# Optimization experiments

Hardware: AMD Instinct MI355X
Metric: run time of the kernel (lower is better)

Reference implementation:

```python
import jax, jax.numpy as jnp
import numpy as np

B, C, P, D = 8192, 1000, 8, 512

def setup_inputs() -> dict:
    key = jax.random.key(0)
    kz, km = jax.random.split(key)
    z = jax.random.normal(kz, (B, D), dtype=jnp.float32)
    mu = jax.random.normal(km, (C, P, D), dtype=jnp.float32)
    return {"z": z, "mu": mu}

def reference(z, mu):
    # Squared Euclidean distance via the GEMM expansion:
    # ||z - mu||^2 = ||z||^2 - 2 z.mu + ||mu||^2  -> [B, C, P]
    z2 = jnp.sum(z * z, axis=-1)          # [B]
    mu2 = jnp.sum(mu * mu, axis=-1)       # [C, P]
    cross = jnp.einsum('bd,cpd->bcp', z, mu)  # [B, C, P]
    dist_sq = z2[:, None, None] - 2.0 * cross + mu2[None, :, :]
    min_dist_sq = jnp.min(dist_sq, axis=2)    # [B, C]
    logits = -min_dist_sq
    return (logits, min_dist_sq)
```

## Files before the change

kernel.cpp:

```cpp
#include <hip/hip_runtime.h>
#include <hip/hip_bf16.h>
#include <stdint.h>
#include <stddef.h>

#define B_ROWS 8192
#define C_CLS  1000
#define NPROTO 8000
#define D_DIM  512

#define TK 64
#define MT 32
#define NT 32

typedef __bf16 bf16x8 __attribute__((ext_vector_type(8)));
typedef float  f32x4  __attribute__((ext_vector_type(4)));

#define AS1 __attribute__((address_space(1)))
#define AS3 __attribute__((address_space(3)))

__device__ __forceinline__ void gload_lds16(const void* g, void* l) {
  __builtin_amdgcn_global_load_lds((const AS1 uint32_t*)g, (AS3 uint32_t*)l, 16, 0, 0);
}

__device__ __forceinline__ f32x4 mfma16(bf16x8 a, bf16x8 b, f32x4 c) {
  return __builtin_amdgcn_mfma_f32_16x16x32_bf16(a, b, c, 0, 0, 0);
}

#define ABUF(d) ((d) * 65536)
#define BBUF(d) ((d) * 65536 + 32768)
#define Z2OFF   131072
#define MU2OFF  132096
#define LDS_BYTES 133120

__global__ void prep_rows(const float* __restrict__ z, const float* __restrict__ mu,
                          __bf16* __restrict__ zb, __bf16* __restrict__ mub,
                          float* __restrict__ z2, float* __restrict__ mu2) {
  const int r = blockIdx.x * 4 + (threadIdx.x >> 6);
  const int l = threadIdx.x & 63;
  const float* src; __bf16* dst; float* sq; int row;
  if (r < B_ROWS) { src = z;  dst = zb;  sq = z2;  row = r; }
  else            { src = mu; dst = mub; sq = mu2; row = r - B_ROWS; }
  const float4* s4 = (const float4*)(src + (size_t)row * D_DIM);
  float4 v0 = s4[l * 2], v1 = s4[l * 2 + 1];
  float ss = v0.x * v0.x + v0.y * v0.y + v0.z * v0.z + v0.w * v0.w
           + v1.x * v1.x + v1.y * v1.y + v1.z * v1.z + v1.w * v1.w;
  bf16x8 o;
  o[0] = (__bf16)v0.x; o[1] = (__bf16)v0.y; o[2] = (__bf16)v0.z; o[3] = (__bf16)v0.w;
  o[4] = (__bf16)v1.x; o[5] = (__bf16)v1.y; o[6] = (__bf16)v1.z; o[7] = (__bf16)v1.w;
  ((bf16x8*)(dst + (size_t)row * D_DIM))[l] = o;
  #pragma unroll
  for (int off = 32; off; off >>= 1) ss += __shfl_down(ss, off);
  if (l == 0) sq[row] = ss;
}

__launch_bounds__(512, 2)
__global__ void proto_gemm(const __bf16* __restrict__ Zb, const __bf16* __restrict__ Mub,
                           const float* __restrict__ Z2, const float* __restrict__ Mu2,
                           float* __restrict__ logits, float* __restrict__ mind) {
  __shared__ __align__(16) unsigned char smem[LDS_BYTES];

  const int tid = threadIdx.x;
  const int l   = tid & 63;
  const int w   = tid >> 6;
  const int wm  = w >> 2;
  const int wn  = w & 3;

  const int xcd = blockIdx.x & 7, cc = blockIdx.x >> 3;
  const int mt = (xcd & 1) * 16 + (cc >> 3);
  const int nt = (xcd >> 1) * 8 + (cc & 7);

  const int sr   = tid >> 3;
  const int scol = ((tid & 7) * 8) ^ ((sr & 7) * 8);
  const __bf16* pA[4]; const __bf16* pB[4];
  #pragma unroll
  for (int q = 0; q < 4; ++q) {
    int rp = mt * 256 + q * 64 + sr;
    if (rp > NPROTO - 1) rp = NPROTO - 1;
    pA[q] = Mub + (size_t)rp * D_DIM + scol;
    pB[q] = Zb + (size_t)(nt * 256 + q * 64 + sr) * D_DIM + scol;
  }
  const int ldst = tid * 16;

  #define STAGE(T, D)                                                        \
    {                                                                        \
      _Pragma("unroll")                                                      \
      for (int q = 0; q < 4; ++q)                                            \
        gload_lds16(pA[q] + (T) * TK, smem + ABUF(D) + q * 8192 + ldst);     \
      _Pragma("unroll")                                                      \
      for (int q = 0; q < 4; ++q)                                            \
        gload_lds16(pB[q] + (T) * TK, smem + BBUF(D) + q * 8192 + ldst);     \
    }

  STAGE(0, 0);
  STAGE(1, 1);

  float* z2s  = (float*)(smem + Z2OFF);
  float* mu2s = (float*)(smem + MU2OFF);
  if (tid < 256) {
    z2s[tid] = Z2[nt * 256 + tid];
  } else {
    const int i = tid - 256;
    const int gp = mt * 256 + i;
    mu2s[i] = Mu2[gp < NPROTO ? gp : NPROTO - 1];
  }

  const int lx = (l & 7) << 4;
  const int lane_lin = (l & 15) * 128 + (l >> 4) * 16;
  const int ok0 = lane_lin ^ lx;
  const int ok1 = (lane_lin + 64) ^ lx;
  const int abase_w = wm * 16384;
  const int bbase_w = wn * 8192;

  f32x4 acc[8][4];
  #pragma unroll
  for (int i = 0; i < 8; ++i)
    #pragma unroll
    for (int j = 0; j < 4; ++j) acc[i][j] = (f32x4){0.f, 0.f, 0.f, 0.f};

  asm volatile("s_waitcnt vmcnt(8)" ::: "memory");
  __builtin_amdgcn_s_barrier();

  #define KTILE(T, DOSTAGE, VMEND)                                               \
  {                                                                              \
    constexpr int d_ = (T) & 1;                                                  \
    const unsigned char* ab = smem + ABUF(d_) + abase_w;                         \
    const unsigned char* bp = smem + BBUF(d_) + bbase_w;                         \
    bf16x8 bb0[4], bb1[4];                                                       \
    _Pragma("unroll")                                                            \
    for (int j = 0; j < 4; ++j) {                                                \
      bb0[j] = *(const bf16x8*)(bp + j * 2048 + ok0);                            \
      bb1[j] = *(const bf16x8*)(bp + j * 2048 + ok1);                            \
    }                                                                            \
    _Pragma("unroll")                                                            \
    for (int ip = 0; ip < 4; ++ip) {                                             \
      bf16x8 a0 = *(const bf16x8*)(ab + (2 * ip) * 2048 + ok0);                  \
      bf16x8 a1 = *(const bf16x8*)(ab + (2 * ip) * 2048 + ok1);                  \
      bf16x8 a2 = *(const bf16x8*)(ab + (2 * ip + 1) * 2048 + ok0);              \
      bf16x8 a3 = *(const bf16x8*)(ab + (2 * ip + 1) * 2048 + ok1);              \
      if (ip == 3 && (DOSTAGE)) {                                                \
        asm volatile("s_waitcnt lgkmcnt(0)" ::: "memory");                       \
        __builtin_amdgcn_s_barrier();                                            \
        STAGE((T) + 2, d_);                                                      \
      }                                                                          \
      __builtin_amdgcn_s_setprio(1);                                             \
      _Pragma("unroll")                                                          \
      for (int j = 0; j < 4; ++j) {                                              \
        acc[2 * ip][j]     = mfma16(a0, bb0[j], acc[2 * ip][j]);                 \
        acc[2 * ip][j]     = mfma16(a1, bb1[j], acc[2 * ip][j]);                 \
        acc[2 * ip + 1][j] = mfma16(a2, bb0[j], acc[2 * ip + 1][j]);             \
        acc[2 * ip + 1][j] = mfma16(a3, bb1[j], acc[2 * ip + 1][j]);             \
      }                                                                          \
      __builtin_amdgcn_s_setprio(0);                                             \
    }                                                                            \
    asm volatile("s_waitcnt vmcnt(" VMEND ")" ::: "memory");                     \
    __builtin_amdgcn_s_barrier();                                                \
  }

  KTILE(0, true, "8")
  KTILE(1, true, "8")
  KTILE(2, true, "8")
  KTILE(3, true, "8")
  KTILE(4, true, "8")
  KTILE(5, true, "8")
  KTILE(6, false, "0")
  KTILE(7, false, "0")

  f32x4 mu2v[8];
  const int rq = l >> 4;
  #pragma unroll
  for (int i = 0; i < 8; ++i)
    mu2v[i] = *(const f32x4*)&mu2s[wm * 128 + i * 16 + rq * 4];

  __syncthreads();
  float* smf = (float*)smem;
  #pragma unroll
  for (int i = 0; i < 8; ++i) {
    const f32x4 m2 = mu2v[i];
    #pragma unroll
    for (int j = 0; j < 4; ++j) {
      const float d0 = fmaf(-2.f, acc[i][j][0], m2[0]);
      const float d1 = fmaf(-2.f, acc[i][j][1], m2[1]);
      const float d2 = fmaf(-2.f, acc[i][j][2], m2[2]);
      const float d3 = fmaf(-2.f, acc[i][j][3], m2[3]);
      float mh = fminf(fminf(d0, d1), fminf(d2, d3));
      float mc = fminf(mh, __shfl_xor(mh, 16));
      if (!(l & 16)) {
        const int zr = wn * 64 + j * 16 + (l & 15);
        const int cl = (wm * 128 + i * 16) / 8 + (l >> 5);
        smf[zr * 36 + cl] = mc;
      }
    }
  }
  __syncthreads();

  const int cb = mt * 32;
  for (int idx = tid; idx < 256 * 8; idx += 512) {
    const int row = idx >> 3, q = idx & 7;
    const int gc = cb + q * 4;
    if (gc < C_CLS) {
      f32x4 v = *(const f32x4*)&smf[row * 36 + q * 4];
      const float zz = z2s[row];
      f32x4 ov = { v[0] + zz, v[1] + zz, v[2] + zz, v[3] + zz };
      const size_t o = (size_t)(nt * 256 + row) * C_CLS + gc;
      *(f32x4*)&mind[o] = ov;
      f32x4 nv = { -ov[0], -ov[1], -ov[2], -ov[3] };
      *(f32x4*)&logits[o] = nv;
    }
  }
}

__global__ void fallback_kernel(const float* __restrict__ z, const float* __restrict__ mu,
                                float* __restrict__ logits, float* __restrict__ mind) {
  const int b = blockIdx.x;
  const int w = threadIdx.x >> 6, l = threadIdx.x & 63;
  const int c = blockIdx.y * 4 + w;
  const float* zr = z + (size_t)b * D_DIM;
  float best = 3.4e38f;
  for (int p = 0; p < 8; ++p) {
    const float* m = mu + ((size_t)c * 8 + p) * D_DIM;
    float s = 0.f;
    for (int d = l; d < D_DIM; d += 64) {
      float df = zr[d] - m[d];
      s = fmaf(df, df, s);
    }
    #pragma unroll
    for (int off = 32; off; off >>= 1) s += __shfl_down(s, off);
    s = __shfl(s, 0);
    best = fminf(best, s);
  }
  if (l == 0) {
    logits[(size_t)b * C_CLS + c] = -best;
    mind[(size_t)b * C_CLS + c] = best;
  }
}

extern "C" void kernel_launch(void* const* d_in, const int* in_sizes, int n_in,
                              void* d_out, int out_size, void* d_ws, size_t ws_size,
                              hipStream_t stream) {
  const float* z  = (const float*)d_in[0];
  const float* mu = (const float*)d_in[1];
  float* logits = (float*)d_out;
  float* mind   = logits + (size_t)B_ROWS * C_CLS;

  const size_t zb_bytes  = (size_t)B_ROWS * D_DIM * 2;
  const size_t mub_bytes = (size_t)NPROTO * D_DIM * 2;
  const size_t need = zb_bytes + mub_bytes + (size_t)B_ROWS * 4 + (size_t)NPROTO * 4;

  if (ws_size >= need) {
    char* p = (char*)d_ws;
    __bf16* zb  = (__bf16*)p; p += zb_bytes;
    __bf16* mub = (__bf16*)p; p += mub_bytes;
    float* z2   = (float*)p;  p += (size_t)B_ROWS * 4;
    float* mu2  = (float*)p;
    prep_rows<<<(B_ROWS + NPROTO) / 4, 256, 0, stream>>>(z, mu, zb, mub, z2, mu2);
    proto_gemm<<<MT * NT, 512, 0, stream>>>(zb, mub, z2, mu2, logits, mind);
  } else {
    dim3 g(B_ROWS, C_CLS / 4);
    fallback_kernel<<<g, 256, 0, stream>>>(z, mu, logits, mind);
  }
}
```

Measured before the change: 155.3 us.

## Split K-tile into barrier-fenced MFMA phases and stage the A and B operands separately

The per-K-tile loop becomes four explicit phases. Each phase loads A fragments, then runs a barrier, an LDS wait and a sched_barrier before a prioritised MFMA burst, and ends with another barrier. The global-to-LDS prefetch is split: the B operand is issued after the first phase and the A operand after the last, so memory traffic is spread across the tile instead of bunched at the end. This aims at a tighter, more predictable MFMA/LDS interleave across waves. In exchange it adds many workgroup barriers per tile, which could stall waves, and it drops the final wait/barrier on the last tile.

```diff
diff --git a/kernel.cpp b/kernel.cpp
--- a/kernel.cpp
+++ b/kernel.cpp
@@ -69,31 +69,6 @@
   const int mt = (xcd & 1) * 16 + (cc >> 3);
   const int nt = (xcd >> 1) * 8 + (cc & 7);
 
-  const int sr   = tid >> 3;
-  const int scol = ((tid & 7) * 8) ^ ((sr & 7) * 8);
-  const __bf16* pA[4]; const __bf16* pB[4];
-  #pragma unroll
-  for (int q = 0; q < 4; ++q) {
-    int rp = mt * 256 + q * 64 + sr;
-    if (rp > NPROTO - 1) rp = NPROTO - 1;
-    pA[q] = Mub + (size_t)rp * D_DIM + scol;
-    pB[q] = Zb + (size_t)(nt * 256 + q * 64 + sr) * D_DIM + scol;
-  }
-  const int ldst = tid * 16;
-
-  #define STAGE(T, D)                                                        \
-    {                                                                        \
-      _Pragma("unroll")                                                      \
-      for (int q = 0; q < 4; ++q)                                            \
-        gload_lds16(pA[q] + (T) * TK, smem + ABUF(D) + q * 8192 + ldst);     \
-      _Pragma("unroll")                                                      \
-      for (int q = 0; q < 4; ++q)                                            \
-        gload_lds16(pB[q] + (T) * TK, smem + BBUF(D) + q * 8192 + ldst);     \
-    }
-
-  STAGE(0, 0);
-  STAGE(1, 1);
-
   float* z2s  = (float*)(smem + Z2OFF);
   float* mu2s = (float*)(smem + MU2OFF);
   if (tid < 256) {
@@ -104,6 +79,30 @@
     mu2s[i] = Mu2[gp < NPROTO ? gp : NPROTO - 1];
   }
 
+  const int sr   = tid >> 3;
+  const int scol = ((tid & 7) * 8) ^ ((sr & 7) * 8);
+  const __bf16* pA[4]; const __bf16* pB[4];
+  #pragma unroll
+  for (int q = 0; q < 4; ++q) {
+    int rp = mt * 256 + q * 64 + sr;
+    if (rp > NPROTO - 1) rp = NPROTO - 1;
+    pA[q] = Mub + (size_t)rp * D_DIM + scol;
+    pB[q] = Zb + (size_t)(nt * 256 + q * 64 + sr) * D_DIM + scol;
+  }
+  const int ldst = tid * 16;
+
+  #define STAGE_A(T, D)                                                      \
+    { _Pragma("unroll")                                                      \
+      for (int q = 0; q < 4; ++q)                                            \
+        gload_lds16(pA[q] + (T) * TK, smem + ABUF(D) + q * 8192 + ldst); }
+  #define STAGE_B(T, D)                                                      \
+    { _Pragma("unroll")                                                      \
+      for (int q = 0; q < 4; ++q)                                            \
+        gload_lds16(pB[q] + (T) * TK, smem + BBUF(D) + q * 8192 + ldst); }
+
+  STAGE_A(0, 0); STAGE_B(0, 0);
+  STAGE_A(1, 1); STAGE_B(1, 1);
+
   const int lx = (l & 7) << 4;
   const int lane_lin = (l & 15) * 128 + (l >> 4) * 16;
   const int ok0 = lane_lin ^ lx;
@@ -120,50 +119,73 @@
   asm volatile("s_waitcnt vmcnt(8)" ::: "memory");
   __builtin_amdgcn_s_barrier();
 
-  #define KTILE(T, DOSTAGE, VMEND)                                               \
+  #define KPHASE(MFMA_I0)                                                        \
+    __builtin_amdgcn_s_barrier();                                                \
+    asm volatile("s_waitcnt lgkmcnt(0)" ::: "memory");                           \
+    __builtin_amdgcn_sched_barrier(0);                                           \
+    __builtin_amdgcn_s_setprio(1);                                               \
+    _Pragma("unroll")                                                            \
+    for (int j = 0; j < 4; ++j) {                                                \
+      acc[MFMA_I0][j]     = mfma16(a0, bb0[j], acc[MFMA_I0][j]);                 \
+      acc[MFMA_I0][j]     = mfma16(a1, bb1[j], acc[MFMA_I0][j]);                 \
+      acc[MFMA_I0 + 1][j] = mfma16(a2, bb0[j], acc[MFMA_I0 + 1][j]);             \
+      acc[MFMA_I0 + 1][j] = mfma16(a3, bb1[j], acc[MFMA_I0 + 1][j]);             \
+    }                                                                            \
+    __builtin_amdgcn_s_setprio(0);                                               \
+    __builtin_amdgcn_s_barrier();
+
+  #define KTILE(T, DOSTAGE, VMEND, DOEND)                                        \
   {                                                                              \
     constexpr int d_ = (T) & 1;                                                  \
     const unsigned char* ab = smem + ABUF(d_) + abase_w;                         \
     const unsigned char* bp = smem + BBUF(d_) + bbase_w;                         \
-    bf16x8 bb0[4], bb1[4];                                                       \
+    bf16x8 bb0[4], bb1[4], a0, a1, a2, a3;                                       \
+                                                          \
     _Pragma("unroll")                                                            \
     for (int j = 0; j < 4; ++j) {                                                \
       bb0[j] = *(const bf16x8*)(bp + j * 2048 + ok0);                            \
       bb1[j] = *(const bf16x8*)(bp + j * 2048 + ok1);                            \
     }                                                                            \
-    _Pragma("unroll")                                                            \
-    for (int ip = 0; ip < 4; ++ip) {                                             \
-      bf16x8 a0 = *(const bf16x8*)(ab + (2 * ip) * 2048 + ok0);                  \
-      bf16x8 a1 = *(const bf16x8*)(ab + (2 * ip) * 2048 + ok1);                  \
-      bf16x8 a2 = *(const bf16x8*)(ab + (2 * ip + 1) * 2048 + ok0);              \
-      bf16x8 a3 = *(const bf16x8*)(ab + (2 * ip + 1) * 2048 + ok1);              \
-      if (ip == 3 && (DOSTAGE)) {                                                \
-        asm volatile("s_waitcnt lgkmcnt(0)" ::: "memory");                       \
-        __builtin_amdgcn_s_barrier();                                            \
-        STAGE((T) + 2, d_);                                                      \
-      }                                                                          \
-      __builtin_amdgcn_s_setprio(1);                                             \
-      _Pragma("unroll")                                                          \
-      for (int j = 0; j < 4; ++j) {                                              \
-        acc[2 * ip][j]     = mfma16(a0, bb0[j], acc[2 * ip][j]);                 \
-        acc[2 * ip][j]     = mfma16(a1, bb1[j], acc[2 * ip][j]);                 \
-        acc[2 * ip + 1][j] = mfma16(a2, bb0[j], acc[2 * ip + 1][j]);             \
-        acc[2 * ip + 1][j] = mfma16(a3, bb1[j], acc[2 * ip + 1][j]);             \
-      }                                                                          \
-      __builtin_amdgcn_s_setprio(0);                                             \
+    a0 = *(const bf16x8*)(ab + 0 * 2048 + ok0);                                  \
+    a1 = *(const bf16x8*)(ab + 0 * 2048 + ok1);                                  \
+    a2 = *(const bf16x8*)(ab + 1 * 2048 + ok0);                                  \
+    a3 = *(const bf16x8*)(ab + 1 * 2048 + ok1);                                  \
+    KPHASE(0)                                                                    \
+                                                   \
+    a0 = *(const bf16x8*)(ab + 2 * 2048 + ok0);                                  \
+    a1 = *(const bf16x8*)(ab + 2 * 2048 + ok1);                                  \
+    a2 = *(const bf16x8*)(ab + 3 * 2048 + ok0);                                  \
+    a3 = *(const bf16x8*)(ab + 3 * 2048 + ok1);                                  \
+    if (DOSTAGE) STAGE_B((T) + 2, d_);                                           \
+    KPHASE(2)                                                                    \
+                                                                  \
+    a0 = *(const bf16x8*)(ab + 4 * 2048 + ok0);                                  \
+    a1 = *(const bf16x8*)(ab + 4 * 2048 + ok1);                                  \
+    a2 = *(const bf16x8*)(ab + 5 * 2048 + ok0);                                  \
+    a3 = *(const bf16x8*)(ab + 5 * 2048 + ok1);                                  \
+    KPHASE(4)                                                                    \
+                                                                  \
+    a0 = *(const bf16x8*)(ab + 6 * 2048 + ok0);                                  \
+    a1 = *(const bf16x8*)(ab + 6 * 2048 + ok1);                                  \
+    a2 = *(const bf16x8*)(ab + 7 * 2048 + ok0);                                  \
+    a3 = *(const bf16x8*)(ab + 7 * 2048 + ok1);                                  \
+    KPHASE(6)                                                                    \
+     \
+    if (DOSTAGE) STAGE_A((T) + 2, d_);                                           \
+    if (DOEND) {                                                                 \
+      asm volatile("s_waitcnt vmcnt(" VMEND ")" ::: "memory");                   \
+      __builtin_amdgcn_s_barrier();                                              \
     }                                                                            \
-    asm volatile("s_waitcnt vmcnt(" VMEND ")" ::: "memory");                     \
-    __builtin_amdgcn_s_barrier();                                                \
-  }
-
-  KTILE(0, true, "8")
-  KTILE(1, true, "8")
-  KTILE(2, true, "8")
-  KTILE(3, true, "8")
-  KTILE(4, true, "8")
-  KTILE(5, true, "8")
-  KTILE(6, false, "0")
-  KTILE(7, false, "0")
+  }
+
+  KTILE(0, true,  "8", true)
+  KTILE(1, true,  "8", true)
+  KTILE(2, true,  "8", true)
+  KTILE(3, true,  "8", true)
+  KTILE(4, true,  "8", true)
+  KTILE(5, true,  "8", true)
+  KTILE(6, false, "0", true)
+  KTILE(7, false, "0", false)
 
   f32x4 mu2v[8];
   const int rq = l >> 4;
```

After: 158.2 us. Within noise of the previous version (+1.9%).
